# Optimization experiments

Hardware: AMD Instinct MI355X
Metric: run time of the kernel (lower is better)

The kernel has to match this reference:

```python
import jax, jax.numpy as jnp
import numpy as np

B, T, D, W, H = 8, 2048, 1024, 16, 8
HD = D // H  # head dim = 128
EPS = 1e-5


def _layernorm(x, g, b):
    m = jnp.mean(x, axis=-1, keepdims=True)
    v = jnp.var(x, axis=-1, keepdims=True)
    return (x - m) / jnp.sqrt(v + EPS) * g + b


def setup_inputs() -> dict:
    key = jax.random.key(0)
    ks = jax.random.split(key, 8)
    s = 0.02
    return {
        "frame_features": jax.random.normal(ks[0], (B, T, D), dtype=jnp.float32),
        "frame_indices": jnp.arange(B * T, dtype=jnp.int64).reshape(B, T),
        # nn.MultiheadAttention packed in-projection (3D, D) and out projection
        "w_qkv": jax.random.normal(ks[1], (3 * D, D), dtype=jnp.float32) * s,
        "b_qkv": jnp.zeros((3 * D,), dtype=jnp.float32),
        "w_out": jax.random.normal(ks[2], (D, D), dtype=jnp.float32) * s,
        "b_out": jnp.zeros((D,), dtype=jnp.float32),
        # FFN: Linear(D, 4D) -> GELU -> Linear(4D, D)
        "w1": jax.random.normal(ks[3], (4 * D, D), dtype=jnp.float32) * s,
        "b1": jnp.zeros((4 * D,), dtype=jnp.float32),
        "w2": jax.random.normal(ks[4], (D, 4 * D), dtype=jnp.float32) * s,
        "b2": jnp.zeros((D,), dtype=jnp.float32),
        "g1": jnp.ones((D,), dtype=jnp.float32),
        "beta1": jnp.zeros((D,), dtype=jnp.float32),
        "g2": jnp.ones((D,), dtype=jnp.float32),
        "beta2": jnp.zeros((D,), dtype=jnp.float32),
    }


def _forward(frame_features, frame_indices, w_qkv, b_qkv, w_out, b_out,
             w1, b1, w2, b2, g1, beta1, g2, beta2):
    # --- sinusoidal temporal positional encoding, indexed by frame number ---
    pos = frame_indices.astype(jnp.float32)[..., None]          # (B, T, 1)
    div = jnp.exp(-jnp.log(10000.0) * jnp.arange(0, D, 2, dtype=jnp.float32) / D)
    ang = pos * div                                              # (B, T, D/2)
    pe = jnp.stack([jnp.sin(ang), jnp.cos(ang)], axis=-1).reshape(B, T, D)
    x = frame_features + pe

    # --- block-diagonal (local window) attention, all windows in one pass ---
    nw = T // W
    xw = x.reshape(B, nw, W, D)
    qkv = jnp.einsum('bnwd,ed->bnwe', xw, w_qkv) + b_qkv         # (B, nw, W, 3D)
    q, k, v = jnp.split(qkv, 3, axis=-1)
    q = q.reshape(B, nw, W, H, HD)
    k = k.reshape(B, nw, W, H, HD)
    v = v.reshape(B, nw, W, H, HD)
    scores = jnp.einsum('bnqhd,bnkhd->bnhqk', q, k) / jnp.sqrt(jnp.float32(HD))
    attn = jax.nn.softmax(scores, axis=-1)
    o = jnp.einsum('bnhqk,bnkhd->bnqhd', attn, v).reshape(B, nw, W, D)
    attn_out = jnp.einsum('bnwd,ed->bnwe', o, w_out) + b_out

    h = _layernorm(xw + attn_out, g1, beta1)
    ffn = jnp.einsum('bnwf,df->bnwd', jax.nn.gelu(
        jnp.einsum('bnwd,fd->bnwf', h, w1) + b1, approximate=False), w2) + b2
    out = _layernorm(h + ffn, g2, beta2)
    return out.reshape(B, T, D)


def reference(frame_features, frame_indices, w_qkv, b_qkv, w_out, b_out,
              w1, b1, w2, b2, g1, beta1, g2, beta2):
    return _forward(frame_features, frame_indices, w_qkv, b_qkv, w_out, b_out,
                    w1, b1, w2, b2, g1, beta1, g2, beta2)
```

## Files before the change

kernel.cpp:

```cpp
#include <hip/hip_runtime.h>
#include <math.h>

typedef __bf16 bf16;
typedef __bf16 bf16x8 __attribute__((ext_vector_type(8)));
typedef __bf16 bf16x4 __attribute__((ext_vector_type(4)));
typedef __bf16 bf16x2 __attribute__((ext_vector_type(2)));
typedef float f32x4 __attribute__((ext_vector_type(4)));

#define ROWS 16384
#define DD   1024

typedef __attribute__((address_space(3))) void* lds_vp;
typedef const __attribute__((address_space(1))) void* glb_vp;
__device__ __forceinline__ void gload16(const void* g, void* l) {
  __builtin_amdgcn_global_load_lds((glb_vp)g, (lds_vp)l, 16, 0, 0);
}

__global__ __launch_bounds__(256) void cast_kernel(
    const float* __restrict__ src, bf16* __restrict__ dst, int n)
{
  int i = (blockIdx.x * 256 + threadIdx.x) * 8;
  if (i >= n) return;
  float4 a = *(const float4*)(src + i);
  float4 b = *(const float4*)(src + i + 4);
  bf16x8 o;
  o[0] = (bf16)a.x; o[1] = (bf16)a.y; o[2] = (bf16)a.z; o[3] = (bf16)a.w;
  o[4] = (bf16)b.x; o[5] = (bf16)b.y; o[6] = (bf16)b.z; o[7] = (bf16)b.w;
  *(bf16x8*)(dst + i) = o;
}

__global__ __launch_bounds__(256) void pe_add_kernel(
    const float* __restrict__ ff, const int* __restrict__ idx, bf16* __restrict__ x)
{
  int p   = blockIdx.x * 256 + threadIdx.x;
  int row = p >> 9;
  int j   = p & 511;
  float pos = (float)idx[row];
  float d2  = (float)(2 * j) * (1.0f / 1024.0f);
  float dv  = expf(-9.210340371976184f * d2);
  float ang = pos * dv;
  float s, c;
  sincosf(ang, &s, &c);
  int base = row * 1024 + 2 * j;
  float2 f = *(const float2*)(ff + base);
  bf16x2 o;
  o[0] = (bf16)(f.x + s);
  o[1] = (bf16)(f.y + c);
  *(bf16x2*)(x + base) = o;
}

template<bool GELU, bool RES>
__global__ __launch_bounds__(256, 2) void gemm_bt(
    const bf16* __restrict__ A, const bf16* __restrict__ Bw,
    const float* __restrict__ bias, const bf16* __restrict__ resid,
    bf16* __restrict__ C, int M, int N, int K)
{
  __shared__ bf16 sA[128 * 32];
  __shared__ bf16 sB[128 * 32];

  const int tid = threadIdx.x;

  int lid = blockIdx.y * gridDim.x + blockIdx.x;
  int xcd = lid & 7;
  int j   = lid >> 3;
  const int bm = (xcd * 16 + (j & 15)) * 128;
  const int bn = (j >> 4) * 128;

  const int wave = tid >> 6;
  const int lane = tid & 63;
  const int wr   = (wave >> 1) * 64;
  const int wc   = (wave & 1) * 64;
  const int ln   = lane & 15;
  const int q    = lane >> 4;

  const int srow = lane >> 2;
  const int sgr  = (lane & 3) * 8;

  f32x4 acc[4][4];
#pragma unroll
  for (int i = 0; i < 4; i++)
#pragma unroll
    for (int jj = 0; jj < 4; jj++) acc[i][jj] = {0.f, 0.f, 0.f, 0.f};

  const bf16* ga0 = A  + (size_t)(bm + wave * 16 + srow) * K + sgr;
  const bf16* ga1 = A  + (size_t)(bm + (wave + 4) * 16 + srow) * K + sgr;
  const bf16* gb0 = Bw + (size_t)(bn + wave * 16 + srow) * K + sgr;
  const bf16* gb1 = Bw + (size_t)(bn + (wave + 4) * 16 + srow) * K + sgr;
  bf16* la0 = &sA[(wave * 16) * 32];
  bf16* la1 = &sA[((wave + 4) * 16) * 32];
  bf16* lb0 = &sB[(wave * 16) * 32];
  bf16* lb1 = &sB[((wave + 4) * 16) * 32];

  for (int k0 = 0; k0 < K; k0 += 32) {
    __syncthreads();
    gload16(ga0 + k0, la0);
    gload16(ga1 + k0, la1);
    gload16(gb0 + k0, lb0);
    gload16(gb1 + k0, lb1);
    __syncthreads();

    bf16x8 af[4], bfr[4];
#pragma unroll
    for (int t = 0; t < 4; t++) {
      af[t]  = *(const bf16x8*)(&sA[(wr + t * 16 + ln) * 32 + q * 8]);
      bfr[t] = *(const bf16x8*)(&sB[(wc + t * 16 + ln) * 32 + q * 8]);
    }
#pragma unroll
    for (int tm = 0; tm < 4; tm++)
#pragma unroll
      for (int tn = 0; tn < 4; tn++)
        acc[tm][tn] = __builtin_amdgcn_mfma_f32_16x16x32_bf16(
            af[tm], bfr[tn], acc[tm][tn], 0, 0, 0);
  }

#pragma unroll
  for (int tm = 0; tm < 4; tm++) {
#pragma unroll
    for (int tn = 0; tn < 4; tn++) {
      int gn = bn + wc + tn * 16 + ln;
      float bv = bias[gn];
#pragma unroll
      for (int i = 0; i < 4; i++) {
        int gm = bm + wr + tm * 16 + q * 4 + i;
        size_t off = (size_t)gm * N + gn;
        float v = acc[tm][tn][i] + bv;
        if (RES) v += (float)resid[off];
        if (GELU) v = 0.5f * v * (1.0f + erff(v * 0.70710678118654752f));
        C[off] = (bf16)v;
      }
    }
  }
}

__global__ __launch_bounds__(256) void attn_kernel(
    const bf16* __restrict__ qkv, bf16* __restrict__ o)
{
  __shared__ float sq[16][132], sk[16][132], sv[16][132];
  __shared__ float ss[16][17];

  int wid = blockIdx.x;
  int h   = wid & 7;
  int win = wid >> 3;
  int tb  = win * 16;

  int t  = threadIdx.x;
  int r  = t >> 4;
  int c8 = (t & 15) * 8;

  const bf16* base = qkv + (size_t)(tb + r) * 3072 + c8;
  bf16x8 qv = *(const bf16x8*)(base + h * 128);
  bf16x8 kv = *(const bf16x8*)(base + 1024 + h * 128);
  bf16x8 vv = *(const bf16x8*)(base + 2048 + h * 128);
#pragma unroll
  for (int u = 0; u < 8; u++) {
    sq[r][c8 + u] = (float)qv[u];
    sk[r][c8 + u] = (float)kv[u];
    sv[r][c8 + u] = (float)vv[u];
  }
  __syncthreads();

  {
    int i = t >> 4, jj = t & 15;
    float s = 0.f;
#pragma unroll 8
    for (int d = 0; d < 128; d++) s += sq[i][d] * sk[jj][d];
    ss[i][jj] = s * 0.08838834764831845f;
  }
  __syncthreads();

  if (t < 16) {
    float m = -1e30f;
    for (int jj = 0; jj < 16; jj++) m = fmaxf(m, ss[t][jj]);
    float sum = 0.f;
    for (int jj = 0; jj < 16; jj++) { float e = expf(ss[t][jj] - m); ss[t][jj] = e; sum += e; }
    float inv = 1.0f / sum;
    for (int jj = 0; jj < 16; jj++) ss[t][jj] *= inv;
  }
  __syncthreads();

  {
    int i = t >> 4; int d0 = (t & 15) * 8;
    float acc[8] = {0, 0, 0, 0, 0, 0, 0, 0};
#pragma unroll
    for (int jj = 0; jj < 16; jj++) {
      float a = ss[i][jj];
#pragma unroll
      for (int u = 0; u < 8; u++) acc[u] += a * sv[jj][d0 + u];
    }
    bf16* op = o + (size_t)(tb + i) * 1024 + h * 128 + d0;
#pragma unroll
    for (int u = 0; u < 8; u++) op[u] = (bf16)acc[u];
  }
}

template<typename OUT_T>
__global__ __launch_bounds__(256) void ln_kernel(
    const bf16* __restrict__ x, const float* __restrict__ g,
    const float* __restrict__ b, OUT_T* __restrict__ y)
{
  __shared__ float red[8];
  int row = blockIdx.x;
  int t   = threadIdx.x;
  int lane = t & 63, wave = t >> 6;

  bf16x4 v4 = *(const bf16x4*)(x + (size_t)row * 1024 + t * 4);
  float v[4];
  float s = 0.f, sq = 0.f;
#pragma unroll
  for (int u = 0; u < 4; u++) {
    v[u] = (float)v4[u];
    s += v[u];
    sq += v[u] * v[u];
  }
  for (int off = 32; off > 0; off >>= 1) {
    s  += __shfl_down(s, off);
    sq += __shfl_down(sq, off);
  }
  if (lane == 0) { red[wave * 2] = s; red[wave * 2 + 1] = sq; }
  __syncthreads();
  float st = red[0] + red[2] + red[4] + red[6];
  float qt = red[1] + red[3] + red[5] + red[7];
  float mean = st * (1.0f / 1024.0f);
  float var  = qt * (1.0f / 1024.0f) - mean * mean;
  float inv  = rsqrtf(var + 1e-5f);
  int c = t * 4;
  OUT_T* yr = y + (size_t)row * 1024 + c;
#pragma unroll
  for (int u = 0; u < 4; u++)
    yr[u] = (OUT_T)((v[u] - mean) * inv * g[c + u] + b[c + u]);
}

extern "C" void kernel_launch(void* const* d_in, const int* in_sizes, int n_in,
                              void* d_out, int out_size, void* d_ws, size_t ws_size,
                              hipStream_t stream) {
  const float* ff    = (const float*)d_in[0];
  const int*   idx   = (const int*)d_in[1];
  const float* w_qkv = (const float*)d_in[2];
  const float* b_qkv = (const float*)d_in[3];
  const float* w_out = (const float*)d_in[4];
  const float* b_out = (const float*)d_in[5];
  const float* w1    = (const float*)d_in[6];
  const float* b1    = (const float*)d_in[7];
  const float* w2    = (const float*)d_in[8];
  const float* b2    = (const float*)d_in[9];
  const float* g1    = (const float*)d_in[10];
  const float* be1   = (const float*)d_in[11];
  const float* g2    = (const float*)d_in[12];
  const float* be2   = (const float*)d_in[13];
  float* out = (float*)d_out;

  char* p = (char*)d_ws;
  bf16* x_bf = (bf16*)p;  p += (size_t)ROWS * 1024 * 2;
  bf16* big  = (bf16*)p;  p += (size_t)ROWS * 4096 * 2;
  bf16* s_bf = (bf16*)p;  p += (size_t)ROWS * 1024 * 2;
  bf16* h_bf = (bf16*)p;  p += (size_t)ROWS * 1024 * 2;
  bf16* wqb  = (bf16*)p;  p += (size_t)3072 * 1024 * 2;
  bf16* wob  = (bf16*)p;  p += (size_t)1024 * 1024 * 2;
  bf16* w1b  = (bf16*)p;  p += (size_t)4096 * 1024 * 2;
  bf16* w2b  = (bf16*)p;  p += (size_t)1024 * 4096 * 2;
  bf16* o_bf = big + (size_t)ROWS * 3072;
  bf16* g_bf = big;

  cast_kernel<<<3072 * 1024 / 8 / 256, 256, 0, stream>>>(w_qkv, wqb, 3072 * 1024);
  cast_kernel<<<1024 * 1024 / 8 / 256, 256, 0, stream>>>(w_out, wob, 1024 * 1024);
  cast_kernel<<<4096 * 1024 / 8 / 256, 256, 0, stream>>>(w1, w1b, 4096 * 1024);
  cast_kernel<<<1024 * 4096 / 8 / 256, 256, 0, stream>>>(w2, w2b, 1024 * 4096);

  pe_add_kernel<<<ROWS * 512 / 256, 256, 0, stream>>>(ff, idx, x_bf);
  gemm_bt<false, false><<<dim3(3072 / 128, ROWS / 128), 256, 0, stream>>>(
      x_bf, wqb, b_qkv, nullptr, big, ROWS, 3072, 1024);
  attn_kernel<<<(ROWS / 16) * 8, 256, 0, stream>>>(big, o_bf);
  gemm_bt<false, true><<<dim3(1024 / 128, ROWS / 128), 256, 0, stream>>>(
      o_bf, wob, b_out, x_bf, s_bf, ROWS, 1024, 1024);
  ln_kernel<bf16><<<ROWS, 256, 0, stream>>>(s_bf, g1, be1, h_bf);
  gemm_bt<true, false><<<dim3(4096 / 128, ROWS / 128), 256, 0, stream>>>(
      h_bf, w1b, b1, nullptr, g_bf, ROWS, 4096, 1024);
  gemm_bt<false, true><<<dim3(1024 / 128, ROWS / 128), 256, 0, stream>>>(
      g_bf, w2b, b2, h_bf, s_bf, ROWS, 1024, 4096);
  ln_kernel<float><<<ROWS, 256, 0, stream>>>(s_bf, g2, be2, out);
}
```

Before: 755.7 us.

## Swizzle GEMM LDS tiles and stage epilogue through LDS for vector stores

```diff
diff --git a/kernel.cpp b/kernel.cpp
--- a/kernel.cpp
+++ b/kernel.cpp
@@ -55,8 +55,9 @@
     const float* __restrict__ bias, const bf16* __restrict__ resid,
     bf16* __restrict__ C, int M, int N, int K)
 {
-  __shared__ bf16 sA[128 * 32];
-  __shared__ bf16 sB[128 * 32];
+  __shared__ bf16 smem[8192];
+  bf16* sA = smem;
+  bf16* sB = smem + 4096;
 
   const int tid = threadIdx.x;
 
@@ -74,7 +75,9 @@
   const int q    = lane >> 4;
 
   const int srow = lane >> 2;
-  const int sgr  = (lane & 3) * 8;
+  const int sgr  = (((lane & 3) ^ ((lane >> 3) & 3))) * 8;
+
+  const int slot = (q ^ ((ln >> 1) & 3)) * 8;
 
   f32x4 acc[4][4];
 #pragma unroll
@@ -102,8 +105,8 @@
     bf16x8 af[4], bfr[4];
 #pragma unroll
     for (int t = 0; t < 4; t++) {
-      af[t]  = *(const bf16x8*)(&sA[(wr + t * 16 + ln) * 32 + q * 8]);
-      bfr[t] = *(const bf16x8*)(&sB[(wc + t * 16 + ln) * 32 + q * 8]);
+      af[t]  = *(const bf16x8*)(&sA[(wr + t * 16 + ln) * 32 + slot]);
+      bfr[t] = *(const bf16x8*)(&sB[(wc + t * 16 + ln) * 32 + slot]);
     }
 #pragma unroll
     for (int tm = 0; tm < 4; tm++)
@@ -113,22 +116,44 @@
             af[tm], bfr[tn], acc[tm][tn], 0, 0, 0);
   }
 
+  const int lr_w = (wave >> 1) * 16 + q * 4;
+  const int lr_r = tid >> 3;
+  const int cb   = (tid & 7) * 16;
 #pragma unroll
   for (int tm = 0; tm < 4; tm++) {
+    __syncthreads();
 #pragma unroll
     for (int tn = 0; tn < 4; tn++) {
       int gn = bn + wc + tn * 16 + ln;
       float bv = bias[gn];
 #pragma unroll
-      for (int i = 0; i < 4; i++) {
-        int gm = bm + wr + tm * 16 + q * 4 + i;
-        size_t off = (size_t)gm * N + gn;
-        float v = acc[tm][tn][i] + bv;
-        if (RES) v += (float)resid[off];
-        if (GELU) v = 0.5f * v * (1.0f + erff(v * 0.70710678118654752f));
-        C[off] = (bf16)v;
+      for (int i = 0; i < 4; i++)
+        smem[(lr_w + i) * 132 + wc + tn * 16 + ln] = (bf16)(acc[tm][tn][i] + bv);
+    }
+    __syncthreads();
+    int gR = bm + (lr_r >> 4) * 64 + tm * 16 + (lr_r & 15);
+    size_t rowoff = (size_t)gR * N + bn + cb;
+    bf16x8 v0 = *(const bf16x8*)&smem[lr_r * 132 + cb];
+    bf16x8 v1 = *(const bf16x8*)&smem[lr_r * 132 + cb + 8];
+    if (RES) {
+      bf16x8 r0 = *(const bf16x8*)(resid + rowoff);
+      bf16x8 r1 = *(const bf16x8*)(resid + rowoff + 8);
+#pragma unroll
+      for (int u = 0; u < 8; u++) {
+        v0[u] = (bf16)((float)v0[u] + (float)r0[u]);
+        v1[u] = (bf16)((float)v1[u] + (float)r1[u]);
       }
     }
+    if (GELU) {
+#pragma unroll
+      for (int u = 0; u < 8; u++) {
+        float a = (float)v0[u], b = (float)v1[u];
+        v0[u] = (bf16)(0.5f * a * (1.0f + erff(a * 0.70710678118654752f)));
+        v1[u] = (bf16)(0.5f * b * (1.0f + erff(b * 0.70710678118654752f)));
+      }
+    }
+    *(bf16x8*)(C + rowoff)     = v0;
+    *(bf16x8*)(C + rowoff + 8) = v1;
   }
 }
 
```

Measured after the change: 747.1 us. No clear change (-1.1%).

## Restructure GEMM: 256x128 tiles, double-buffered A in LDS, B fragments from registers

Applied to the files above, without the earlier changes.

```diff
diff --git a/kernel.cpp b/kernel.cpp
--- a/kernel.cpp
+++ b/kernel.cpp
@@ -8,7 +8,6 @@
 typedef float f32x4 __attribute__((ext_vector_type(4)));
 
 #define ROWS 16384
-#define DD   1024
 
 typedef __attribute__((address_space(3))) void* lds_vp;
 typedef const __attribute__((address_space(1))) void* glb_vp;
@@ -55,80 +54,120 @@
     const float* __restrict__ bias, const bf16* __restrict__ resid,
     bf16* __restrict__ C, int M, int N, int K)
 {
-  __shared__ bf16 sA[128 * 32];
-  __shared__ bf16 sB[128 * 32];
+  __shared__ bf16 smem[16384];
+  bf16* bufA0 = smem;
+  bf16* bufA1 = smem + 8192;
 
   const int tid = threadIdx.x;
 
   int lid = blockIdx.y * gridDim.x + blockIdx.x;
   int xcd = lid & 7;
   int j   = lid >> 3;
-  const int bm = (xcd * 16 + (j & 15)) * 128;
-  const int bn = (j >> 4) * 128;
+  const int bm = (xcd * 8 + (j & 7)) * 256;
+  const int bn = (j >> 3) * 128;
 
   const int wave = tid >> 6;
   const int lane = tid & 63;
-  const int wr   = (wave >> 1) * 64;
-  const int wc   = (wave & 1) * 64;
+  const int wr   = wave * 64;
   const int ln   = lane & 15;
   const int q    = lane >> 4;
 
   const int srow = lane >> 2;
-  const int sgr  = (lane & 3) * 8;
-
-  f32x4 acc[4][4];
-#pragma unroll
-  for (int i = 0; i < 4; i++)
-#pragma unroll
-    for (int jj = 0; jj < 4; jj++) acc[i][jj] = {0.f, 0.f, 0.f, 0.f};
-
-  const bf16* ga0 = A  + (size_t)(bm + wave * 16 + srow) * K + sgr;
-  const bf16* ga1 = A  + (size_t)(bm + (wave + 4) * 16 + srow) * K + sgr;
-  const bf16* gb0 = Bw + (size_t)(bn + wave * 16 + srow) * K + sgr;
-  const bf16* gb1 = Bw + (size_t)(bn + (wave + 4) * 16 + srow) * K + sgr;
-  bf16* la0 = &sA[(wave * 16) * 32];
-  bf16* la1 = &sA[((wave + 4) * 16) * 32];
-  bf16* lb0 = &sB[(wave * 16) * 32];
-  bf16* lb1 = &sB[((wave + 4) * 16) * 32];
-
-  for (int k0 = 0; k0 < K; k0 += 32) {
+  const int sgr  = ((lane & 3) ^ ((lane >> 3) & 3)) * 8;
+  const int slot = (q ^ ((ln >> 1) & 3)) * 8;
+
+  const bf16* gA = A + (size_t)(bm + wave * 16 + srow) * K + sgr;
+  const bf16* pB = Bw + (size_t)(bn + ln) * K + q * 8;
+
+  f32x4 acc[4][8];
+#pragma unroll
+  for (int tm = 0; tm < 4; tm++)
+#pragma unroll
+    for (int tn = 0; tn < 8; tn++) acc[tm][tn] = {0.f, 0.f, 0.f, 0.f};
+
+  bf16x8 b0[8], b1[8];
+
+#define DMAA(buf, kk)                                                         \
+  {                                                                           \
+    _Pragma("unroll") for (int c = 0; c < 4; c++)                             \
+        gload16(gA + (size_t)(c * 64) * K + (kk),                             \
+                &buf[(c * 64 + wave * 16) * 32]);                             \
+  }
+#define LOADB(dst, kk)                                                        \
+  {                                                                           \
+    _Pragma("unroll") for (int tn = 0; tn < 8; tn++)                          \
+        dst[tn] = *(const bf16x8*)(pB + (size_t)(tn * 16) * K + (kk));        \
+  }
+#define COMPUTE(buf, bv)                                                      \
+  {                                                                           \
+    bf16x8 af[4];                                                             \
+    _Pragma("unroll") for (int tm = 0; tm < 4; tm++)                          \
+        af[tm] = *(const bf16x8*)(&buf[(wr + tm * 16 + ln) * 32 + slot]);     \
+    _Pragma("unroll") for (int tm = 0; tm < 4; tm++)                          \
+        _Pragma("unroll") for (int tn = 0; tn < 8; tn++)                      \
+            acc[tm][tn] = __builtin_amdgcn_mfma_f32_16x16x32_bf16(            \
+                af[tm], bv[tn], acc[tm][tn], 0, 0, 0);                        \
+  }
+
+  DMAA(bufA0, 0);
+  LOADB(b0, 0);
+
+  for (int k0 = 0; k0 < K; k0 += 64) {
     __syncthreads();
-    gload16(ga0 + k0, la0);
-    gload16(ga1 + k0, la1);
-    gload16(gb0 + k0, lb0);
-    gload16(gb1 + k0, lb1);
+    DMAA(bufA1, k0 + 32);
+    LOADB(b1, k0 + 32);
+    COMPUTE(bufA0, b0);
     __syncthreads();
-
-    bf16x8 af[4], bfr[4];
-#pragma unroll
-    for (int t = 0; t < 4; t++) {
-      af[t]  = *(const bf16x8*)(&sA[(wr + t * 16 + ln) * 32 + q * 8]);
-      bfr[t] = *(const bf16x8*)(&sB[(wc + t * 16 + ln) * 32 + q * 8]);
+    if (k0 + 64 < K) {
+      DMAA(bufA0, k0 + 64);
+      LOADB(b0, k0 + 64);
     }
-#pragma unroll
-    for (int tm = 0; tm < 4; tm++)
-#pragma unroll
-      for (int tn = 0; tn < 4; tn++)
-        acc[tm][tn] = __builtin_amdgcn_mfma_f32_16x16x32_bf16(
-            af[tm], bfr[tn], acc[tm][tn], 0, 0, 0);
-  }
-
+    COMPUTE(bufA1, b1);
+  }
+#undef DMAA
+#undef LOADB
+#undef COMPUTE
+
+  float bv[8];
+#pragma unroll
+  for (int tn = 0; tn < 8; tn++) bv[tn] = bias[bn + tn * 16 + ln];
+
+  const int s_  = tid >> 2;
+  const int cb  = (tid & 3) * 32;
 #pragma unroll
   for (int tm = 0; tm < 4; tm++) {
-#pragma unroll
-    for (int tn = 0; tn < 4; tn++) {
-      int gn = bn + wc + tn * 16 + ln;
-      float bv = bias[gn];
-#pragma unroll
-      for (int i = 0; i < 4; i++) {
-        int gm = bm + wr + tm * 16 + q * 4 + i;
-        size_t off = (size_t)gm * N + gn;
-        float v = acc[tm][tn][i] + bv;
-        if (RES) v += (float)resid[off];
-        if (GELU) v = 0.5f * v * (1.0f + erff(v * 0.70710678118654752f));
-        C[off] = (bf16)v;
+    __syncthreads();
+#pragma unroll
+    for (int tn = 0; tn < 8; tn++)
+#pragma unroll
+      for (int i = 0; i < 4; i++)
+        smem[(wave * 16 + q * 4 + i) * 132 + tn * 16 + ln] =
+            (bf16)(acc[tm][tn][i] + bv[tn]);
+    __syncthreads();
+    int gR = bm + (s_ >> 4) * 64 + tm * 16 + (s_ & 15);
+    size_t rowoff = (size_t)gR * N + bn + cb;
+    bf16x8 v[4];
+#pragma unroll
+    for (int u = 0; u < 4; u++) v[u] = *(const bf16x8*)&smem[s_ * 132 + cb + u * 8];
+    if (RES) {
+#pragma unroll
+      for (int u = 0; u < 4; u++) {
+        bf16x8 r = *(const bf16x8*)(resid + rowoff + u * 8);
+#pragma unroll
+        for (int e = 0; e < 8; e++) v[u][e] = (bf16)((float)v[u][e] + (float)r[e]);
       }
     }
+    if (GELU) {
+#pragma unroll
+      for (int u = 0; u < 4; u++)
+#pragma unroll
+        for (int e = 0; e < 8; e++) {
+          float a = (float)v[u][e];
+          v[u][e] = (bf16)(0.5f * a * (1.0f + erff(a * 0.70710678118654752f)));
+        }
+    }
+#pragma unroll
+    for (int u = 0; u < 4; u++) *(bf16x8*)(C + rowoff + u * 8) = v[u];
   }
 }
 
@@ -267,15 +306,15 @@
   cast_kernel<<<1024 * 4096 / 8 / 256, 256, 0, stream>>>(w2, w2b, 1024 * 4096);
 
   pe_add_kernel<<<ROWS * 512 / 256, 256, 0, stream>>>(ff, idx, x_bf);
-  gemm_bt<false, false><<<dim3(3072 / 128, ROWS / 128), 256, 0, stream>>>(
+  gemm_bt<false, false><<<dim3(3072 / 128, 64), 256, 0, stream>>>(
       x_bf, wqb, b_qkv, nullptr, big, ROWS, 3072, 1024);
   attn_kernel<<<(ROWS / 16) * 8, 256, 0, stream>>>(big, o_bf);
-  gemm_bt<false, true><<<dim3(1024 / 128, ROWS / 128), 256, 0, stream>>>(
+  gemm_bt<false, true><<<dim3(1024 / 128, 64), 256, 0, stream>>>(
       o_bf, wob, b_out, x_bf, s_bf, ROWS, 1024, 1024);
   ln_kernel<bf16><<<ROWS, 256, 0, stream>>>(s_bf, g1, be1, h_bf);
-  gemm_bt<true, false><<<dim3(4096 / 128, ROWS / 128), 256, 0, stream>>>(
+  gemm_bt<true, false><<<dim3(4096 / 128, 64), 256, 0, stream>>>(
       h_bf, w1b, b1, nullptr, g_bf, ROWS, 4096, 1024);
-  gemm_bt<false, true><<<dim3(1024 / 128, ROWS / 128), 256, 0, stream>>>(
+  gemm_bt<false, true><<<dim3(1024 / 128, 64), 256, 0, stream>>>(
       g_bf, w2b, b2, h_bf, s_bf, ROWS, 1024, 4096);
   ln_kernel<float><<<ROWS, 256, 0, stream>>>(s_bf, g2, be2, out);
 }
```

Result: slower. 1.256 ms (+66.3%).
